# Optimization experiments

Measured on AMD Instinct MI355X. Metric: run time of the kernel, lower is better.

The kernel has to match this reference:

```python
import jax, jax.numpy as jnp
import numpy as np

L, H, DH = 6, 16, 96          # depth, heads, dim_head
DIM = 1024
INNER = H * DH                # 1536
DFF = 4 * DIM                 # ff_mult * dim
NLAT = 128                    # num_latents
EPS = 1e-5


def _ln(x, g, b):
    mu = jnp.mean(x, axis=-1, keepdims=True)
    xc = x - mu
    var = jnp.mean(xc * xc, axis=-1, keepdims=True)
    return xc * jax.lax.rsqrt(var + EPS) * g + b


def setup_inputs() -> dict:
    key = jax.random.key(0)
    ks = jax.random.split(key, 10)
    b, T, F, v = 8, 4, 1, 1024
    s = 0.02
    return {
        "x": jax.random.normal(ks[0], (b, T, F, v, DIM), jnp.float32),
        "vision_attn_masks": jax.random.randint(ks[1], (b, F * v), 0, 2).astype(jnp.float32),
        "latents": jax.random.normal(ks[2], (NLAT, DIM), jnp.float32),  # nn.Parameter(randn)
        "ln_m_g": jnp.ones((L, DIM), jnp.float32),
        "ln_m_b": jnp.zeros((L, DIM), jnp.float32),
        "ln_l_g": jnp.ones((L, DIM), jnp.float32),
        "ln_l_b": jnp.zeros((L, DIM), jnp.float32),
        "q_w": jax.random.normal(ks[3], (L, DIM, INNER), jnp.float32) * s,
        "kv_w": jax.random.normal(ks[4], (L, DIM, 2 * INNER), jnp.float32) * s,
        "out_w": jax.random.normal(ks[5], (L, INNER, DIM), jnp.float32) * s,
        "ff_ln_g": jnp.ones((L, DIM), jnp.float32),
        "ff_ln_b": jnp.zeros((L, DIM), jnp.float32),
        "ff_w1": jax.random.normal(ks[6], (L, DIM, DFF), jnp.float32) * s,
        "ff_w2": jax.random.normal(ks[7], (L, DFF, DIM), jnp.float32) * s,
        "fn_g": jnp.ones((DIM,), jnp.float32),
        "fn_b": jnp.zeros((DIM,), jnp.float32),
    }


def reference(x, vision_attn_masks, latents, ln_m_g, ln_m_b, ln_l_g, ln_l_b,
              q_w, kv_w, out_w, ff_ln_g, ff_ln_b, ff_w1, ff_w2, fn_g, fn_b):
    b, T, F, v, D = x.shape
    scale = DH ** -0.5
    x = x.reshape(b, T, F * v, D)                      # (b,T,n1,D)
    lat = jnp.broadcast_to(latents, (b, T, NLAT, D))   # (b,T,n2,D)
    # mask over KV axis: media tokens per vision_attn_masks, latents always valid
    mask = jnp.concatenate(
        [vision_attn_masks, jnp.ones((b, NLAT), vision_attn_masks.dtype)], axis=-1)
    bias = jnp.where(mask > 0, 0.0, -jnp.inf)[:, None, None, None, :]  # (b,1,1,1,Nkv)
    for i in range(L):
        xm = _ln(x, ln_m_g[i], ln_m_b[i])
        lm = _ln(lat, ln_l_g[i], ln_l_b[i])
        q = (lm @ q_w[i]).reshape(b, T, NLAT, H, DH) * scale
        kvin = jnp.concatenate([xm, lm], axis=-2)       # (b,T,Nkv,D)
        N = kvin.shape[-2]
        k, vv = jnp.split(kvin @ kv_w[i], 2, axis=-1)
        k = k.reshape(b, T, N, H, DH)
        vv = vv.reshape(b, T, N, H, DH)
        sim = jnp.einsum('btihd,btjhd->bhtij', q, k) + bias
        attn = jax.nn.softmax(sim, axis=-1)             # max-subtract softmax
        o = jnp.einsum('bhtij,btjhd->btihd', attn, vv).reshape(b, T, NLAT, INNER)
        lat = lat + o @ out_w[i]                        # attn residual
        hdn = jax.nn.gelu(_ln(lat, ff_ln_g[i], ff_ln_b[i]) @ ff_w1[i], approximate=False)
        lat = lat + hdn @ ff_w2[i]                      # FFN residual
    return _ln(lat, fn_g, fn_b)
```

## Files before the change

### kernel.cpp

```cpp
#include <hip/hip_runtime.h>


typedef __attribute__((ext_vector_type(8))) short bf16x8;
typedef __attribute__((ext_vector_type(4))) float f32x4;
typedef unsigned int u32;
typedef unsigned short u16;

#define MFMA16(a, b, c) __builtin_amdgcn_mfma_f32_16x16x32_bf16((a), (b), (c), 0, 0, 0)

__device__ __forceinline__ u16 f2bf(float f) {
  u32 u = __builtin_bit_cast(u32, f);
  u = (u + 0x7fffu + ((u >> 16) & 1u)) >> 16;
  return (u16)u;
}

__device__ __forceinline__ void gld_lds16(const void* g, void* l) {
  __builtin_amdgcn_global_load_lds(
      (const __attribute__((address_space(1))) u32*)g,
      (__attribute__((address_space(3))) u32*)l, 16, 0, 0);
}

__global__ __launch_bounds__(256) void maskscan(const float* __restrict__ vm,
                                                int* __restrict__ dest,
                                                int* __restrict__ cnt,
                                                int* __restrict__ cntp) {
  const int b = blockIdx.x, t = threadIdx.x;
  int v[4], s = 0;
#pragma unroll
  for (int i = 0; i < 4; ++i) {
    v[i] = vm[b * 1024 + t * 4 + i] > 0.f ? 1 : 0;
    s += v[i];
  }
  const int lane = t & 63, w = t >> 6;
  int ps = s;
#pragma unroll
  for (int d = 1; d < 64; d <<= 1) {
    int o = __shfl_up(ps, d);
    if (lane >= d) ps += o;
  }
  __shared__ int wsum[4];
  if (lane == 63) wsum[w] = ps;
  __syncthreads();
  int wb = 0;
  for (int i = 0; i < w; ++i) wb += wsum[i];
  int base = wb + ps - s;
#pragma unroll
  for (int i = 0; i < 4; ++i) {
    dest[b * 1024 + t * 4 + i] = v[i] ? base : -1;
    base += v[i];
  }
  if (t == 255) {
    const int tot = wb + ps;
    cnt[b] = tot;
    cntp[b] = (tot + 127) & ~127;
  }
}

__global__ void tilebuild(const int* __restrict__ cntp, int* __restrict__ tileRows,
                          int* __restrict__ tileCnt) {
  if (threadIdx.x != 0 || blockIdx.x != 0) return;
  int n = 0;
  for (int bt = 0; bt < 32; ++bt) {
    const int nt = cntp[bt >> 2] >> 7;
    for (int j = 0; j < nt; ++j) tileRows[n++] = bt * 1152 + j * 128;
  }
  *tileCnt = n;
}

__global__ __launch_bounds__(256) void init_lat(const float* __restrict__ latents,
                                                float* __restrict__ lat) {
  const int r = blockIdx.x;
  ((float4*)(lat + (size_t)r * 1024))[threadIdx.x] =
      ((const float4*)(latents + (size_t)(r & 127) * 1024))[threadIdx.x];
}

__global__ __launch_bounds__(256) void wcastT(const float* __restrict__ W,
                                              u16* __restrict__ WT, int K, int N,
                                              float scale,
                                              const float* __restrict__ gk) {
  __shared__ float tile[32][33];
  const int tx = threadIdx.x & 31;
  const int ty = threadIdx.x >> 5;
  const int n0 = blockIdx.x * 32;
  const int k0 = blockIdx.y * 32;
#pragma unroll
  for (int i = 0; i < 4; ++i) {
    const int kk = k0 + ty + i * 8;
    float w = W[(size_t)kk * N + n0 + tx];
    if (gk) w *= gk[kk];
    tile[ty + i * 8][tx] = w;
  }
  __syncthreads();
#pragma unroll
  for (int i = 0; i < 4; ++i)
    WT[(size_t)(n0 + ty + i * 8) * K + k0 + tx] = f2bf(tile[tx][ty + i * 8] * scale);
}

__global__ __launch_bounds__(256) void zero3072(float* __restrict__ r) {
  r[blockIdx.x * 256 + threadIdx.x] = 0.f;
}
__global__ __launch_bounds__(256) void biasrow2(const float* __restrict__ bvec,
                                                const float* __restrict__ W,
                                                float* __restrict__ r) {
  const int n = blockIdx.x * 256 + threadIdx.x;
  const int k0 = blockIdx.y * 64;
  float acc = 0.f;
#pragma unroll 8
  for (int k = 0; k < 64; ++k) acc += bvec[k0 + k] * W[(size_t)(k0 + k) * 3072 + n];
  atomicAdd(&r[n], acc);
}

__global__ __launch_bounds__(256) void ln0_gather(const float* __restrict__ x,
                                                  const int* __restrict__ dest,
                                                  u16* __restrict__ kvin) {
  const int r = blockIdx.x;
  const int bt = r >> 10, tok = r & 1023, b = bt >> 2;
  const int di = dest[b * 1024 + tok];
  if (di < 0) return;
  const int t = threadIdx.x;
  float4 xv = ((const float4*)(x + (size_t)r * 1024))[t];
  float s = xv.x + xv.y + xv.z + xv.w;
  float s2 = xv.x * xv.x + xv.y * xv.y + xv.z * xv.z + xv.w * xv.w;
#pragma unroll
  for (int d = 1; d < 64; d <<= 1) {
    s += __shfl_xor(s, d);
    s2 += __shfl_xor(s2, d);
  }
  __shared__ float red[8];
  const int w = t >> 6;
  if ((t & 63) == 0) {
    red[w] = s;
    red[4 + w] = s2;
  }
  __syncthreads();
  s = red[0] + red[1] + red[2] + red[3];
  s2 = red[4] + red[5] + red[6] + red[7];
  const float mu = s * (1.f / 1024.f);
  const float rs = rsqrtf(fmaxf(s2 * (1.f / 1024.f) - mu * mu, 0.f) + 1e-5f);
  ushort4 o;
  o.x = f2bf((xv.x - mu) * rs);
  o.y = f2bf((xv.y - mu) * rs);
  o.z = f2bf((xv.z - mu) * rs);
  o.w = f2bf((xv.w - mu) * rs);
  ((ushort4*)(kvin + ((size_t)bt * 1152 + di) * 1024))[t] = o;
}

__global__ __launch_bounds__(256) void ln1024_bf16(
    const float* __restrict__ in, const float* __restrict__ g,
    const float* __restrict__ b, u16* __restrict__ out1, int grp, int stride,
    int off, u16* __restrict__ out2) {
  const int r = blockIdx.x;
  const int t = threadIdx.x;
  float4 xv = ((const float4*)(in + (size_t)r * 1024))[t];
  float s = xv.x + xv.y + xv.z + xv.w;
  float s2 = xv.x * xv.x + xv.y * xv.y + xv.z * xv.z + xv.w * xv.w;
#pragma unroll
  for (int d = 1; d < 64; d <<= 1) {
    s += __shfl_xor(s, d);
    s2 += __shfl_xor(s2, d);
  }
  __shared__ float red[8];
  const int w = t >> 6;
  if ((t & 63) == 0) {
    red[w] = s;
    red[4 + w] = s2;
  }
  __syncthreads();
  s = red[0] + red[1] + red[2] + red[3];
  s2 = red[4] + red[5] + red[6] + red[7];
  const float mu = s * (1.f / 1024.f);
  const float rs = rsqrtf(fmaxf(s2 * (1.f / 1024.f) - mu * mu, 0.f) + 1e-5f);
  float4 gv = ((const float4*)g)[t];
  float4 bv = ((const float4*)b)[t];
  ushort4 o;
  o.x = f2bf((xv.x - mu) * rs * gv.x + bv.x);
  o.y = f2bf((xv.y - mu) * rs * gv.y + bv.y);
  o.z = f2bf((xv.z - mu) * rs * gv.z + bv.z);
  o.w = f2bf((xv.w - mu) * rs * gv.w + bv.w);
  const size_t orow = (size_t)(r / grp) * stride + off + (r % grp);
  ((ushort4*)(out1 + orow * 1024))[t] = o;
  if (out2) ((ushort4*)(out2 + (size_t)r * 1024))[t] = o;
}

__global__ __launch_bounds__(256) void red4_ln(
    const float* __restrict__ part, float* __restrict__ lat,
    const float* __restrict__ g, const float* __restrict__ b,
    u16* __restrict__ out1, int grp, int stride, int off,
    u16* __restrict__ out2, float* __restrict__ outf) {
  const int r = blockIdx.x;
  const int t = threadIdx.x;
  float4 xv = ((const float4*)(lat + (size_t)r * 1024))[t];
#pragma unroll
  for (int z = 0; z < 4; ++z) {
    float4 pz = ((const float4*)(part + (size_t)z * 4194304 + (size_t)r * 1024))[t];
    xv.x += pz.x; xv.y += pz.y; xv.z += pz.z; xv.w += pz.w;
  }
  ((float4*)(lat + (size_t)r * 1024))[t] = xv;
  float s = xv.x + xv.y + xv.z + xv.w;
  float s2 = xv.x * xv.x + xv.y * xv.y + xv.z * xv.z + xv.w * xv.w;
#pragma unroll
  for (int d = 1; d < 64; d <<= 1) {
    s += __shfl_xor(s, d);
    s2 += __shfl_xor(s2, d);
  }
  __shared__ float red[8];
  const int w = t >> 6;
  if ((t & 63) == 0) {
    red[w] = s;
    red[4 + w] = s2;
  }
  __syncthreads();
  s = red[0] + red[1] + red[2] + red[3];
  s2 = red[4] + red[5] + red[6] + red[7];
  const float mu = s * (1.f / 1024.f);
  const float rs = rsqrtf(fmaxf(s2 * (1.f / 1024.f) - mu * mu, 0.f) + 1e-5f);
  float4 gv = ((const float4*)g)[t];
  float4 bv = ((const float4*)b)[t];
  float4 o;
  o.x = (xv.x - mu) * rs * gv.x + bv.x;
  o.y = (xv.y - mu) * rs * gv.y + bv.y;
  o.z = (xv.z - mu) * rs * gv.z + bv.z;
  o.w = (xv.w - mu) * rs * gv.w + bv.w;
  if (out1) {
    ushort4 ob;
    ob.x = f2bf(o.x); ob.y = f2bf(o.y); ob.z = f2bf(o.z); ob.w = f2bf(o.w);
    const size_t orow = (size_t)(r / grp) * stride + off + (r % grp);
    ((ushort4*)(out1 + orow * 1024))[t] = ob;
    if (out2) ((ushort4*)(out2 + (size_t)r * 1024))[t] = ob;
  }
  if (outf) ((float4*)(outf + (size_t)r * 1024))[t] = o;
}

__global__ __launch_bounds__(256) void gemm_bt(
    const u16* __restrict__ A, const u16* __restrict__ BT, int N, int K, int mode,
    void* __restrict__ out0, void* __restrict__ out1, void* __restrict__ out2,
    const float* __restrict__ rbias, const int* __restrict__ tileRows,
    const int* __restrict__ tileCnt, int Ksplit) {
  int m0;
  if (tileRows) {
    if ((int)blockIdx.y >= *tileCnt) return;
    m0 = tileRows[blockIdx.y];
  } else {
    m0 = blockIdx.y * 128;
  }
  __shared__ u16 Alds[2 * 128 * 32];
  __shared__ u16 Blds[2 * 128 * 32];
  const int t = threadIdx.x;
  const int l = t & 63;
  const int w = t >> 6;
  const int n0 = blockIdx.x * 128;
  const int wr = (w >> 1) * 64;
  const int wc = (w & 1) * 64;
  const int srow = t >> 2;
  const int scol = (t & 3) * 8;
  const int frow = l & 15;
  const int fk = (l >> 4) * 8;

  f32x4 acc[4][4] = {};

  const u16* Ab = A + (size_t)(m0 + srow) * K + scol;
  const u16* Bb = BT + (size_t)(n0 + srow) * K + scol;
  const size_t r64K = (size_t)64 * K;

  const int koff = blockIdx.z * Ksplit;
  for (int k0 = koff; k0 < koff + Ksplit; k0 += 64) {
    __syncthreads();
    gld_lds16(Ab + k0, &Alds[t * 8]);
    gld_lds16(Ab + r64K + k0, &Alds[2048 + t * 8]);
    gld_lds16(Ab + k0 + 32, &Alds[4096 + t * 8]);
    gld_lds16(Ab + r64K + k0 + 32, &Alds[6144 + t * 8]);
    gld_lds16(Bb + k0, &Blds[t * 8]);
    gld_lds16(Bb + r64K + k0, &Blds[2048 + t * 8]);
    gld_lds16(Bb + k0 + 32, &Blds[4096 + t * 8]);
    gld_lds16(Bb + r64K + k0 + 32, &Blds[6144 + t * 8]);
    __syncthreads();
#pragma unroll
    for (int ph = 0; ph < 2; ++ph) {
      bf16x8 af[4], bfr[4];
#pragma unroll
      for (int i = 0; i < 4; ++i)
        af[i] = *(const bf16x8*)&Alds[ph * 4096 + (wr + i * 16 + frow) * 32 + fk];
#pragma unroll
      for (int j = 0; j < 4; ++j)
        bfr[j] = *(const bf16x8*)&Blds[ph * 4096 + (wc + j * 16 + frow) * 32 + fk];
#pragma unroll
      for (int i = 0; i < 4; ++i)
#pragma unroll
        for (int j = 0; j < 4; ++j) acc[i][j] = MFMA16(af[i], bfr[j], acc[i][j]);
    }
  }

  const int col = l & 15;
  const int r4 = (l >> 4) * 4;
  const int btq = m0 / 1152;
  const int nbase = m0 - btq * 1152;
#pragma unroll
  for (int i = 0; i < 4; ++i) {
    const int roff = wr + i * 16 + r4;
    const int row0 = m0 + roff;
#pragma unroll
    for (int j = 0; j < 4; ++j) {
      const int c = n0 + wc + j * 16 + col;
      if (mode == 3) {
        const float bc = rbias[c];
        if (c < 1536) {
          u16* Kb = (u16*)out0;
#pragma unroll
          for (int r = 0; r < 4; ++r)
            Kb[(size_t)(row0 + r) * 1536 + c] = f2bf(acc[i][j][r] + bc);
        } else {
          const int cc = c - 1536;
          const int hh = cc / 96, dd = cc - hh * 96;
          ushort4 pk;
          pk.x = f2bf(acc[i][j][0] + bc);
          pk.y = f2bf(acc[i][j][1] + bc);
          pk.z = f2bf(acc[i][j][2] + bc);
          pk.w = f2bf(acc[i][j][3] + bc);
          *(ushort4*)((u16*)out1 +
                      ((size_t)(btq * 16 + hh) * 96 + dd) * 1152 + nbase + roff) = pk;
        }
      } else if (mode == 4) {
        const int bt = row0 >> 7, ii = row0 & 127;
        if (c < 1536) {
          u16* Qb = (u16*)out0;
#pragma unroll
          for (int r = 0; r < 4; ++r)
            Qb[(size_t)(row0 + r) * 1536 + c] = f2bf(acc[i][j][r]);
        } else if (c < 3072) {
          u16* Kb = (u16*)out1;
#pragma unroll
          for (int r = 0; r < 4; ++r)
            Kb[((size_t)bt * 1152 + 1024 + ii + r) * 1536 + (c - 1536)] =
                f2bf(acc[i][j][r]);
        } else {
          const int cc = c - 3072;
          const int hh = cc / 96, dd = cc - hh * 96;
          ushort4 pk;
          pk.x = f2bf(acc[i][j][0]);
          pk.y = f2bf(acc[i][j][1]);
          pk.z = f2bf(acc[i][j][2]);
          pk.w = f2bf(acc[i][j][3]);
          *(ushort4*)((u16*)out2 +
                      ((size_t)(bt * 16 + hh) * 96 + dd) * 1152 + 1024 + ii) = pk;
        }
      } else if (mode == 5) {
        float* O = (float*)out0 + (size_t)blockIdx.z * 4194304;
#pragma unroll
        for (int r = 0; r < 4; ++r) O[(size_t)(row0 + r) * N + c] = acc[i][j][r];
      } else {
        u16* O = (u16*)out0;
#pragma unroll
        for (int r = 0; r < 4; ++r) {
          float v = acc[i][j][r];
          if (mode == 1) v = 0.5f * v * (1.f + erff(v * 0.70710678118f));
          O[(size_t)(row0 + r) * N + c] = f2bf(v);
        }
      }
    }
  }
}

__global__ __launch_bounds__(256) void attn_kernel(
    const u16* __restrict__ Q, const u16* __restrict__ Kb,
    const u16* __restrict__ Vt, const int* __restrict__ cnt_d,
    const int* __restrict__ cntp_d, u16* __restrict__ O) {
  const int bh = blockIdx.x;
  const int bt = bh >> 4;
  const int h = bh & 15;
  const int bb = bt >> 2;
  const int t = threadIdx.x, l = t & 63, w = t >> 6;
  const int lr = l & 15, lg = l >> 4;

  const int cnt = cnt_d[bb];
  const int nchunks = 1 + (cntp_d[bb] >> 7);

  __shared__ u16 Plds[4][32 * 136];

  bf16x8 qf[2][3];
#pragma unroll
  for (int mt = 0; mt < 2; ++mt)
#pragma unroll
    for (int ks = 0; ks < 3; ++ks)
      qf[mt][ks] = *(const bf16x8*)(Q +
          (size_t)(bt * 128 + w * 32 + mt * 16 + lr) * 1536 + h * 96 + ks * 32 + lg * 8);

  f32x4 oa[2][6] = {};
  float m_i[2][4], l_i[2][4];
#pragma unroll
  for (int mt = 0; mt < 2; ++mt)
#pragma unroll
    for (int r = 0; r < 4; ++r) {
      m_i[mt][r] = -1e30f;
      l_i[mt][r] = 0.f;
    }

  const float L2E = 1.44269504088896f;
  u16* myP = &Plds[w][0];

  for (int ci = 0; ci < nchunks; ++ci) {
    const int nb = (ci == 0) ? 1024 : (ci - 1) * 128;

    f32x4 s[2][8];
#pragma unroll
    for (int nt = 0; nt < 8; ++nt) {
      f32x4 s0 = {}, s1 = {};
      const u16* kp =
          Kb + (size_t)(bt * 1152 + nb + nt * 16 + lr) * 1536 + h * 96 + lg * 8;
#pragma unroll
      for (int ks = 0; ks < 3; ++ks) {
        bf16x8 kf = *(const bf16x8*)(kp + ks * 32);
        s0 = MFMA16(qf[0][ks], kf, s0);
        s1 = MFMA16(qf[1][ks], kf, s1);
      }
      const float bn =
          (nb >= 1024) ? 0.f : (((nb + nt * 16 + lr) < cnt) ? 0.f : -1e30f);
      s[0][nt] = s0 + bn;
      s[1][nt] = s1 + bn;
    }

    float alpha[2][4];
#pragma unroll
    for (int mt = 0; mt < 2; ++mt)
#pragma unroll
      for (int r = 0; r < 4; ++r) {
        float mx = s[mt][0][r];
#pragma unroll
        for (int nt = 1; nt < 8; ++nt) mx = fmaxf(mx, s[mt][nt][r]);
#pragma unroll
        for (int d = 1; d < 16; d <<= 1) mx = fmaxf(mx, __shfl_xor(mx, d));
        const float mn = fmaxf(m_i[mt][r], mx);
        alpha[mt][r] = exp2f((m_i[mt][r] - mn) * L2E);
        m_i[mt][r] = mn;
      }

#pragma unroll
    for (int mt = 0; mt < 2; ++mt) {
      float rsum[4] = {0.f, 0.f, 0.f, 0.f};
#pragma unroll
      for (int nt = 0; nt < 8; ++nt)
#pragma unroll
        for (int r = 0; r < 4; ++r) {
          const float pv = exp2f((s[mt][nt][r] - m_i[mt][r]) * L2E);
          rsum[r] += pv;
          myP[(mt * 16 + 4 * lg + r) * 136 + nt * 16 + lr] = f2bf(pv);
        }
#pragma unroll
      for (int r = 0; r < 4; ++r) {
        float rs = rsum[r];
#pragma unroll
        for (int d = 1; d < 16; d <<= 1) rs += __shfl_xor(rs, d);
        l_i[mt][r] = alpha[mt][r] * l_i[mt][r] + rs;
      }
    }

#pragma unroll
    for (int mt = 0; mt < 2; ++mt)
#pragma unroll
      for (int dt = 0; dt < 6; ++dt)
#pragma unroll
        for (int r = 0; r < 4; ++r) oa[mt][dt][r] *= alpha[mt][r];

    __syncthreads();

#pragma unroll
    for (int dt = 0; dt < 6; ++dt) {
      const u16* vp = Vt + ((size_t)bh * 96 + dt * 16 + lr) * 1152 + nb + lg * 8;
#pragma unroll
      for (int ks = 0; ks < 4; ++ks) {
        bf16x8 vf = *(const bf16x8*)(vp + ks * 32);
        bf16x8 p0 = *(const bf16x8*)&myP[lr * 136 + ks * 32 + lg * 8];
        bf16x8 p1 = *(const bf16x8*)&myP[(16 + lr) * 136 + ks * 32 + lg * 8];
        oa[0][dt] = MFMA16(p0, vf, oa[0][dt]);
        oa[1][dt] = MFMA16(p1, vf, oa[1][dt]);
      }
    }
    __syncthreads();
  }

#pragma unroll
  for (int mt = 0; mt < 2; ++mt)
#pragma unroll
    for (int r = 0; r < 4; ++r) {
      const float inv = 1.f / l_i[mt][r];
#pragma unroll
      for (int dt = 0; dt < 6; ++dt)
        O[(size_t)(bt * 128 + w * 32 + mt * 16 + 4 * lg + r) * 1536 + h * 96 +
          dt * 16 + lr] = f2bf(oa[mt][dt][r] * inv);
    }
}

extern "C" void kernel_launch(void* const* d_in, const int* in_sizes, int n_in,
                              void* d_out, int out_size, void* d_ws, size_t ws_size,
                              hipStream_t stream) {
  const float* x = (const float*)d_in[0];
  const float* vmask = (const float*)d_in[1];
  const float* latents = (const float*)d_in[2];
  const float* ln_m_g = (const float*)d_in[3];
  const float* ln_m_b = (const float*)d_in[4];
  const float* ln_l_g = (const float*)d_in[5];
  const float* ln_l_b = (const float*)d_in[6];
  const float* q_w = (const float*)d_in[7];
  const float* kv_w = (const float*)d_in[8];
  const float* out_w = (const float*)d_in[9];
  const float* ff_ln_g = (const float*)d_in[10];
  const float* ff_ln_b = (const float*)d_in[11];
  const float* ff_w1 = (const float*)d_in[12];
  const float* ff_w2 = (const float*)d_in[13];
  const float* fn_g = (const float*)d_in[14];
  const float* fn_b = (const float*)d_in[15];

  char* p = (char*)d_ws;
  auto alloc = [&](size_t n) {
    char* r = p;
    p += (n + 255) & ~(size_t)255;
    return r;
  };
  u16* kvin = (u16*)alloc((size_t)36864 * 1024 * 2);
  u16* lmq = (u16*)alloc((size_t)4096 * 1024 * 2);
  u16* qbuf = (u16*)alloc((size_t)4096 * 1536 * 2);
  u16* Kbuf = (u16*)alloc((size_t)36864 * 1536 * 2);
  u16* Vtb = (u16*)alloc((size_t)512 * 96 * 1152 * 2);
  u16* obuf = (u16*)alloc((size_t)4096 * 1536 * 2);
  float* lat = (float*)alloc((size_t)4096 * 1024 * 4);
  u16* kvwTm = (u16*)alloc((size_t)3072 * 1024 * 2);
  u16* qkvT = (u16*)alloc((size_t)4608 * 1024 * 2);
  u16* outwT = (u16*)alloc((size_t)1024 * 1536 * 2);
  u16* ffw1T = (u16*)alloc((size_t)4096 * 1024 * 2);
  u16* ffw2T = (u16*)alloc((size_t)1024 * 4096 * 2);
  float* rbias = (float*)alloc(3072 * 4);
  int* dest = (int*)alloc(8192 * 4);
  int* cntd = (int*)alloc(64);
  int* cntp = (int*)alloc(64);
  int* tileRows = (int*)alloc(260 * 4);
  int* tileCnt = (int*)alloc(4);
  u16* latln = lmq;
  u16* ffh = Vtb;
  float* part = (float*)Kbuf;
  (void)in_sizes; (void)n_in; (void)out_size; (void)ws_size;

  maskscan<<<8, 256, 0, stream>>>(vmask, dest, cntd, cntp);
  tilebuild<<<1, 1, 0, stream>>>(cntp, tileRows, tileCnt);
  ln0_gather<<<32768, 256, 0, stream>>>(x, dest, kvin);
  init_lat<<<4096, 256, 0, stream>>>(latents, lat);
  ln1024_bf16<<<4096, 256, 0, stream>>>(lat, ln_l_g, ln_l_b, kvin, 128, 1152, 1024, lmq);

  const float qscale = 0.10206207261596577f;

  for (int L = 0; L < 6; ++L) {
    wcastT<<<dim3(96, 32), 256, 0, stream>>>(kv_w + (size_t)L * 1024 * 3072, kvwTm,
                                             1024, 3072, 1.f, ln_m_g + L * 1024);
    zero3072<<<12, 256, 0, stream>>>(rbias);
    biasrow2<<<dim3(12, 16), 256, 0, stream>>>(ln_m_b + L * 1024,
                                               kv_w + (size_t)L * 1024 * 3072, rbias);
    wcastT<<<dim3(48, 32), 256, 0, stream>>>(q_w + (size_t)L * 1024 * 1536, qkvT,
                                             1024, 1536, qscale, nullptr);
    wcastT<<<dim3(96, 32), 256, 0, stream>>>(kv_w + (size_t)L * 1024 * 3072,
                                             qkvT + (size_t)1536 * 1024, 1024, 3072,
                                             1.f, nullptr);
    wcastT<<<dim3(32, 48), 256, 0, stream>>>(out_w + (size_t)L * 1536 * 1024, outwT,
                                             1536, 1024, 1.f, nullptr);
    wcastT<<<dim3(128, 32), 256, 0, stream>>>(ff_w1 + (size_t)L * 1024 * 4096, ffw1T,
                                              1024, 4096, 1.f, nullptr);
    wcastT<<<dim3(32, 128), 256, 0, stream>>>(ff_w2 + (size_t)L * 4096 * 1024, ffw2T,
                                              4096, 1024, 1.f, nullptr);

    gemm_bt<<<dim3(24, 256), 256, 0, stream>>>(kvin, kvwTm, 3072, 1024, 3, Kbuf, Vtb,
                                               nullptr, rbias, tileRows, tileCnt, 1024);
    gemm_bt<<<dim3(36, 32), 256, 0, stream>>>(lmq, qkvT, 4608, 1024, 4, qbuf, Kbuf,
                                              Vtb, nullptr, nullptr, nullptr, 1024);
    attn_kernel<<<512, 256, 0, stream>>>(qbuf, Kbuf, Vtb, cntd, cntp, obuf);
    gemm_bt<<<dim3(8, 32, 4), 256, 0, stream>>>(obuf, outwT, 1024, 1536, 5, part,
                                                nullptr, nullptr, nullptr, nullptr,
                                                nullptr, 384);
    red4_ln<<<4096, 256, 0, stream>>>(part, lat, ff_ln_g + L * 1024,
                                      ff_ln_b + L * 1024, latln, 4096, 0, 0,
                                      nullptr, nullptr);
    gemm_bt<<<dim3(32, 32), 256, 0, stream>>>(latln, ffw1T, 4096, 1024, 1, ffh,
                                              nullptr, nullptr, nullptr, nullptr,
                                              nullptr, 1024);
    gemm_bt<<<dim3(8, 32, 4), 256, 0, stream>>>(ffh, ffw2T, 1024, 4096, 5, part,
                                                nullptr, nullptr, nullptr, nullptr,
                                                nullptr, 1024);
    if (L < 5) {
      red4_ln<<<4096, 256, 0, stream>>>(part, lat, ln_l_g + (L + 1) * 1024,
                                        ln_l_b + (L + 1) * 1024, kvin, 128, 1152,
                                        1024, lmq, nullptr);
    } else {
      red4_ln<<<4096, 256, 0, stream>>>(part, lat, fn_g, fn_b, nullptr, 1, 0, 0,
                                        nullptr, (float*)d_out);
    }
  }
}
```

Measured before the change: 4.514 ms.

## Template GEMM on mode, halve K-step LDS tile, and fuse weight casts

The GEMM kernel becomes a template on its epilogue mode so dead branches compile away. The K step per LDS stage drops from 64 to 32, which halves shared memory, and launch bounds now request 4 blocks per SM to raise occupancy. In exchange there are twice as many barrier-separated load/compute iterations. Four separate weight transpose-cast launches per layer are also merged into one wcast4 kernel to cut launch overhead.

```diff
diff --git a/kernel.cpp b/kernel.cpp
--- a/kernel.cpp
+++ b/kernel.cpp
@@ -94,6 +94,45 @@
 #pragma unroll
   for (int i = 0; i < 4; ++i)
     WT[(size_t)(n0 + ty + i * 8) * K + k0 + tx] = f2bf(tile[tx][ty + i * 8] * scale);
+}
+
+__global__ __launch_bounds__(256) void wcast4(const float* __restrict__ kv_w,
+                                              const float* __restrict__ q_w,
+                                              const float* __restrict__ ff_w1,
+                                              const float* __restrict__ g,
+                                              float qscale, u16* __restrict__ kvwTm,
+                                              u16* __restrict__ qkvT,
+                                              u16* __restrict__ ffw1T) {
+  const int nt = blockIdx.x;
+  const float* W;
+  u16* D;
+  int N, n0;
+  const float* gk = nullptr;
+  float sc = 1.f;
+  if (nt < 96) {
+    W = kv_w; D = kvwTm; N = 3072; n0 = nt * 32; gk = g;
+  } else if (nt < 144) {
+    W = q_w; D = qkvT; N = 1536; n0 = (nt - 96) * 32; sc = qscale;
+  } else if (nt < 240) {
+    W = kv_w; D = qkvT + (size_t)1536 * 1024; N = 3072; n0 = (nt - 144) * 32;
+  } else {
+    W = ff_w1; D = ffw1T; N = 4096; n0 = (nt - 240) * 32;
+  }
+  __shared__ float tile[32][33];
+  const int tx = threadIdx.x & 31;
+  const int ty = threadIdx.x >> 5;
+  const int k0 = blockIdx.y * 32;
+#pragma unroll
+  for (int i = 0; i < 4; ++i) {
+    const int kk = k0 + ty + i * 8;
+    float w = W[(size_t)kk * N + n0 + tx];
+    if (gk) w *= gk[kk];
+    tile[ty + i * 8][tx] = w;
+  }
+  __syncthreads();
+#pragma unroll
+  for (int i = 0; i < 4; ++i)
+    D[(size_t)(n0 + ty + i * 8) * 1024 + k0 + tx] = f2bf(tile[tx][ty + i * 8] * sc);
 }
 
 __global__ __launch_bounds__(256) void zero3072(float* __restrict__ r) {
@@ -231,8 +270,9 @@
   if (outf) ((float4*)(outf + (size_t)r * 1024))[t] = o;
 }
 
-__global__ __launch_bounds__(256) void gemm_bt(
-    const u16* __restrict__ A, const u16* __restrict__ BT, int N, int K, int mode,
+template <int MODE>
+__global__ __launch_bounds__(256, 4) void gemm_bt(
+    const u16* __restrict__ A, const u16* __restrict__ BT, int N, int K,
     void* __restrict__ out0, void* __restrict__ out1, void* __restrict__ out2,
     const float* __restrict__ rbias, const int* __restrict__ tileRows,
     const int* __restrict__ tileCnt, int Ksplit) {
@@ -243,8 +283,8 @@
   } else {
     m0 = blockIdx.y * 128;
   }
-  __shared__ u16 Alds[2 * 128 * 32];
-  __shared__ u16 Blds[2 * 128 * 32];
+  __shared__ u16 Alds[128 * 32];
+  __shared__ u16 Blds[128 * 32];
   const int t = threadIdx.x;
   const int l = t & 63;
   const int w = t >> 6;
@@ -258,36 +298,30 @@
 
   f32x4 acc[4][4] = {};
 
-  const u16* Ab = A + (size_t)(m0 + srow) * K + scol;
-  const u16* Bb = BT + (size_t)(n0 + srow) * K + scol;
-  const size_t r64K = (size_t)64 * K;
+  const u16* Ap = A + (size_t)(m0 + srow) * K + scol;
+  const u16* Ap2 = Ap + (size_t)64 * K;
+  const u16* Bp = BT + (size_t)(n0 + srow) * K + scol;
+  const u16* Bp2 = Bp + (size_t)64 * K;
 
   const int koff = blockIdx.z * Ksplit;
-  for (int k0 = koff; k0 < koff + Ksplit; k0 += 64) {
+  for (int k0 = koff; k0 < koff + Ksplit; k0 += 32) {
     __syncthreads();
-    gld_lds16(Ab + k0, &Alds[t * 8]);
-    gld_lds16(Ab + r64K + k0, &Alds[2048 + t * 8]);
-    gld_lds16(Ab + k0 + 32, &Alds[4096 + t * 8]);
-    gld_lds16(Ab + r64K + k0 + 32, &Alds[6144 + t * 8]);
-    gld_lds16(Bb + k0, &Blds[t * 8]);
-    gld_lds16(Bb + r64K + k0, &Blds[2048 + t * 8]);
-    gld_lds16(Bb + k0 + 32, &Blds[4096 + t * 8]);
-    gld_lds16(Bb + r64K + k0 + 32, &Blds[6144 + t * 8]);
+    gld_lds16(Ap + k0, &Alds[t * 8]);
+    gld_lds16(Ap2 + k0, &Alds[2048 + t * 8]);
+    gld_lds16(Bp + k0, &Blds[t * 8]);
+    gld_lds16(Bp2 + k0, &Blds[2048 + t * 8]);
     __syncthreads();
-#pragma unroll
-    for (int ph = 0; ph < 2; ++ph) {
-      bf16x8 af[4], bfr[4];
-#pragma unroll
-      for (int i = 0; i < 4; ++i)
-        af[i] = *(const bf16x8*)&Alds[ph * 4096 + (wr + i * 16 + frow) * 32 + fk];
-#pragma unroll
-      for (int j = 0; j < 4; ++j)
-        bfr[j] = *(const bf16x8*)&Blds[ph * 4096 + (wc + j * 16 + frow) * 32 + fk];
-#pragma unroll
-      for (int i = 0; i < 4; ++i)
-#pragma unroll
-        for (int j = 0; j < 4; ++j) acc[i][j] = MFMA16(af[i], bfr[j], acc[i][j]);
-    }
+    bf16x8 af[4], bfr[4];
+#pragma unroll
+    for (int i = 0; i < 4; ++i)
+      af[i] = *(const bf16x8*)&Alds[(wr + i * 16 + frow) * 32 + fk];
+#pragma unroll
+    for (int j = 0; j < 4; ++j)
+      bfr[j] = *(const bf16x8*)&Blds[(wc + j * 16 + frow) * 32 + fk];
+#pragma unroll
+    for (int i = 0; i < 4; ++i)
+#pragma unroll
+      for (int j = 0; j < 4; ++j) acc[i][j] = MFMA16(af[i], bfr[j], acc[i][j]);
   }
 
   const int col = l & 15;
@@ -301,7 +335,7 @@
 #pragma unroll
     for (int j = 0; j < 4; ++j) {
       const int c = n0 + wc + j * 16 + col;
-      if (mode == 3) {
+      if constexpr (MODE == 3) {
         const float bc = rbias[c];
         if (c < 1536) {
           u16* Kb = (u16*)out0;
@@ -319,7 +353,7 @@
           *(ushort4*)((u16*)out1 +
                       ((size_t)(btq * 16 + hh) * 96 + dd) * 1152 + nbase + roff) = pk;
         }
-      } else if (mode == 4) {
+      } else if constexpr (MODE == 4) {
         const int bt = row0 >> 7, ii = row0 & 127;
         if (c < 1536) {
           u16* Qb = (u16*)out0;
@@ -343,7 +377,7 @@
           *(ushort4*)((u16*)out2 +
                       ((size_t)(bt * 16 + hh) * 96 + dd) * 1152 + 1024 + ii) = pk;
         }
-      } else if (mode == 5) {
+      } else if constexpr (MODE == 5) {
         float* O = (float*)out0 + (size_t)blockIdx.z * 4194304;
 #pragma unroll
         for (int r = 0; r < 4; ++r) O[(size_t)(row0 + r) * N + c] = acc[i][j][r];
@@ -352,7 +386,7 @@
 #pragma unroll
         for (int r = 0; r < 4; ++r) {
           float v = acc[i][j][r];
-          if (mode == 1) v = 0.5f * v * (1.f + erff(v * 0.70710678118f));
+          if constexpr (MODE == 1) v = 0.5f * v * (1.f + erff(v * 0.70710678118f));
           O[(size_t)(row0 + r) * N + c] = f2bf(v);
         }
       }
@@ -547,40 +581,37 @@
   const float qscale = 0.10206207261596577f;
 
   for (int L = 0; L < 6; ++L) {
-    wcastT<<<dim3(96, 32), 256, 0, stream>>>(kv_w + (size_t)L * 1024 * 3072, kvwTm,
-                                             1024, 3072, 1.f, ln_m_g + L * 1024);
+    wcast4<<<dim3(368, 32), 256, 0, stream>>>(kv_w + (size_t)L * 1024 * 3072,
+                                              q_w + (size_t)L * 1024 * 1536,
+                                              ff_w1 + (size_t)L * 1024 * 4096,
+                                              ln_m_g + L * 1024, qscale, kvwTm,
+                                              qkvT, ffw1T);
     zero3072<<<12, 256, 0, stream>>>(rbias);
     biasrow2<<<dim3(12, 16), 256, 0, stream>>>(ln_m_b + L * 1024,
                                                kv_w + (size_t)L * 1024 * 3072, rbias);
-    wcastT<<<dim3(48, 32), 256, 0, stream>>>(q_w + (size_t)L * 1024 * 1536, qkvT,
-                                             1024, 1536, qscale, nullptr);
-    wcastT<<<dim3(96, 32), 256, 0, stream>>>(kv_w + (size_t)L * 1024 * 3072,
-                                             qkvT + (size_t)1536 * 1024, 1024, 3072,
-                                             1.f, nullptr);
     wcastT<<<dim3(32, 48), 256, 0, stream>>>(out_w + (size_t)L * 1536 * 1024, outwT,
                                              1536, 1024, 1.f, nullptr);
-    wcastT<<<dim3(128, 32), 256, 0, stream>>>(ff_w1 + (size_t)L * 1024 * 4096, ffw1T,
-                                              1024, 4096, 1.f, nullptr);
     wcastT<<<dim3(32, 128), 256, 0, stream>>>(ff_w2 + (size_t)L * 4096 * 1024, ffw2T,
                                               4096, 1024, 1.f, nullptr);
 
-    gemm_bt<<<dim3(24, 256), 256, 0, stream>>>(kvin, kvwTm, 3072, 1024, 3, Kbuf, Vtb,
-                                               nullptr, rbias, tileRows, tileCnt, 1024);
-    gemm_bt<<<dim3(36, 32), 256, 0, stream>>>(lmq, qkvT, 4608, 1024, 4, qbuf, Kbuf,
-                                              Vtb, nullptr, nullptr, nullptr, 1024);
+    gemm_bt<3><<<dim3(24, 256), 256, 0, stream>>>(kvin, kvwTm, 3072, 1024, Kbuf, Vtb,
+                                                  nullptr, rbias, tileRows, tileCnt,
+                                                  1024);
+    gemm_bt<4><<<dim3(36, 32), 256, 0, stream>>>(lmq, qkvT, 4608, 1024, qbuf, Kbuf,
+                                                 Vtb, nullptr, nullptr, nullptr, 1024);
     attn_kernel<<<512, 256, 0, stream>>>(qbuf, Kbuf, Vtb, cntd, cntp, obuf);
-    gemm_bt<<<dim3(8, 32, 4), 256, 0, stream>>>(obuf, outwT, 1024, 1536, 5, part,
-                                                nullptr, nullptr, nullptr, nullptr,
-                                                nullptr, 384);
+    gemm_bt<5><<<dim3(8, 32, 4), 256, 0, stream>>>(obuf, outwT, 1024, 1536, part,
+                                                   nullptr, nullptr, nullptr, nullptr,
+                                                   nullptr, 384);
     red4_ln<<<4096, 256, 0, stream>>>(part, lat, ff_ln_g + L * 1024,
                                       ff_ln_b + L * 1024, latln, 4096, 0, 0,
                                       nullptr, nullptr);
-    gemm_bt<<<dim3(32, 32), 256, 0, stream>>>(latln, ffw1T, 4096, 1024, 1, ffh,
-                                              nullptr, nullptr, nullptr, nullptr,
-                                              nullptr, 1024);
-    gemm_bt<<<dim3(8, 32, 4), 256, 0, stream>>>(ffh, ffw2T, 1024, 4096, 5, part,
-                                                nullptr, nullptr, nullptr, nullptr,
-                                                nullptr, 1024);
+    gemm_bt<1><<<dim3(32, 32), 256, 0, stream>>>(latln, ffw1T, 4096, 1024, ffh,
+                                                 nullptr, nullptr, nullptr, nullptr,
+                                                 nullptr, 1024);
+    gemm_bt<5><<<dim3(8, 32, 4), 256, 0, stream>>>(ffh, ffw2T, 1024, 4096, part,
+                                                   nullptr, nullptr, nullptr, nullptr,
+                                                   nullptr, 1024);
     if (L < 5) {
       red4_ln<<<4096, 256, 0, stream>>>(part, lat, ln_l_g + (L + 1) * 1024,
                                         ln_l_b + (L + 1) * 1024, kvin, 128, 1152,
```

Result: faster. 3.768 ms (-16.5%).
